# Kernel tuning notes

Hardware: AMD Instinct MI355X
Metric: run time of the kernel (lower is better)

The kernel has to match this reference:

```python
import jax, jax.numpy as jnp
import numpy as np

NUM_SAMPLES = 8192   # num_parallel_samples
HIDDEN = 512
EMB = 40             # embedding_dim(10) * freq_map['H'](4)
C_IN = 1
TIME_FEAT = 4
HIST_LEN = 336
PRED_LEN = 48
MIN_SCALE = 1e-5
SAMPLE_KEY_SEED = 42


def _gru_cell(h, x, W_ih, W_hh, b_ih, b_hh):
    # torch GRU cell: gates stacked as [r, z, n] along rows of W (each HIDDEN)
    gi = x @ W_ih.T + b_ih            # [B, 3H]
    gh = h @ W_hh.T + b_hh            # [B, 3H]
    H = h.shape[-1]
    i_r, i_z, i_n = gi[:, :H], gi[:, H:2 * H], gi[:, 2 * H:]
    h_r, h_z, h_n = gh[:, :H], gh[:, H:2 * H], gh[:, 2 * H:]
    r = jax.nn.sigmoid(i_r + h_r)
    z = jax.nn.sigmoid(i_z + h_z)
    n = jnp.tanh(i_n + r * h_n)
    return (1.0 - z) * n + z * h


def setup_inputs() -> dict:
    key = jax.random.key(0)
    ks = jax.random.split(key, 16)
    f32 = jnp.float32
    inp = {
        "x": jax.random.normal(ks[0], (1, HIST_LEN, C_IN), dtype=f32),
        "x_mark": jax.random.normal(ks[1], (1, HIST_LEN, TIME_FEAT), dtype=f32),
        "y_mark": jax.random.normal(ks[2], (1, PRED_LEN, TIME_FEAT), dtype=f32),
        "mode": 0,
        # time_feat_embedding: Linear(4 -> 40), torch layout [out, in]
        "W_emb": jax.random.normal(ks[3], (EMB, TIME_FEAT), dtype=f32) * 0.05,
        "b_emb": jnp.zeros((EMB,), dtype=f32),
        # GRU (1 layer): input size = c_in + EMB = 41
        "W_ih": jax.random.normal(ks[4], (3 * HIDDEN, C_IN + EMB), dtype=f32) * 0.05,
        "W_hh": jax.random.normal(ks[5], (3 * HIDDEN, HIDDEN), dtype=f32) * 0.05,
        "b_ih": jnp.zeros((3 * HIDDEN,), dtype=f32),
        "b_hh": jnp.zeros((3 * HIDDEN,), dtype=f32),
        # StudentT args projection: three Linear(HIDDEN -> 1)
        "W_df": jax.random.normal(ks[6], (1, HIDDEN), dtype=f32) * 0.05,
        "b_df": jnp.zeros((1,), dtype=f32),
        "W_loc": jax.random.normal(ks[7], (1, HIDDEN), dtype=f32) * 0.05,
        "b_loc": jnp.zeros((1,), dtype=f32),
        "W_sc": jax.random.normal(ks[8], (1, HIDDEN), dtype=f32) * 0.05,
        "b_sc": jnp.zeros((1,), dtype=f32),
    }
    return inp


def _deepar_sample(x, x_mark, y_mark, W_emb, b_emb, W_ih, W_hh, b_ih, b_hh,
                   W_df, b_df, W_loc, b_loc, W_sc, b_sc):
    S = NUM_SAMPLES
    # ---- encoder (unroll_encoder with y=None) ----
    scale = jnp.clip(jnp.mean(jnp.abs(x), axis=1, keepdims=True), MIN_SCALE, None)  # [1,1,1]
    seq = x / scale
    tfe = x_mark @ W_emb.T + b_emb                      # [1, T, EMB]
    enc_in = jnp.concatenate([seq, tfe], axis=-1)       # [1, T, 41]
    h0 = jnp.zeros((1, HIDDEN), dtype=x.dtype)

    def enc_step(h, xt):  # xt: [1, 41]
        h = _gru_cell(h, xt, W_ih, W_hh, b_ih, b_hh)
        return h, None

    h_T, _ = jax.lax.scan(enc_step, h0, jnp.swapaxes(enc_in, 0, 1))  # [1, H]

    # ---- sampling decoder ----
    h = jnp.broadcast_to(h_T, (S, HIDDEN))              # repeat state across samples
    # note: original feeds the UNSCALED last observation as first decoder input
    tgt0 = jnp.broadcast_to(x[0, -1, :], (S, C_IN))     # [S, 1]
    emb_y = y_mark[0] @ W_emb.T + b_emb                 # [pred_len, EMB]
    scale_s = scale[0, 0, 0]                            # scalar (batch=1, c=1)
    base_key = jax.random.key(SAMPLE_KEY_SEED)

    def dec_step(carry, xs):
        h, tgt = carry
        e_k, k = xs
        inp = jnp.concatenate([tgt, jnp.broadcast_to(e_k, (S, EMB))], axis=-1)  # [S, 41]
        h = _gru_cell(h, inp, W_ih, W_hh, b_ih, b_hh)
        # StudentTOutput domain map: df = 2 + softplus, loc raw, scale = softplus
        df = 2.0 + jax.nn.softplus(h @ W_df.T + b_df)   # [S, 1]
        loc = h @ W_loc.T + b_loc                       # [S, 1]
        sc = jax.nn.softplus(h @ W_sc.T + b_sc)         # [S, 1]
        eps = jax.random.t(jax.random.fold_in(base_key, k),
                           jax.lax.stop_gradient(df), df.shape, dtype=df.dtype)
        sample = (loc + sc * eps) * scale_s             # AffineTransformed(scale)
        return (h, sample), sample

    ks = jnp.arange(PRED_LEN)
    _, samples = jax.lax.scan(dec_step, (h, tgt0), (emb_y, ks))  # [pred_len, S, 1]
    return jnp.transpose(samples, (1, 0, 2))            # [S, pred_len, c_out]


def reference(x, x_mark, y_mark, mode, W_emb, b_emb, W_ih, W_hh, b_ih, b_hh,
              W_df, b_df, W_loc, b_loc, W_sc, b_sc):
    # mode=0 -> sampling/inference path (the kernel target)
    return _deepar_sample(x, x_mark, y_mark, W_emb, b_emb, W_ih, W_hh, b_ih, b_hh,
                          W_df, b_df, W_loc, b_loc, W_sc, b_sc)
```

## Files before the change

### kernel.cpp

```cpp
#include <hip/hip_runtime.h>
#include <cmath>


#define JAX_PARTITIONABLE 1

#define HIDDEN 512
#define EMB 40
#define HIST 336
#define PRED 48
#define S_N 8192
#define ENC_BLOCKS 48

#define HPLANE (8192 * 512)
#define WPLANE (1536 * 512)
#define INV4096 (1.0f / 4096.0f)

typedef __attribute__((ext_vector_type(8))) _Float16 half8;
typedef __attribute__((ext_vector_type(4))) float f32x4;

struct KeyPair { unsigned a, b; };

__device__ __forceinline__ unsigned rotl32_(unsigned v, unsigned s) {
  return (v << s) | (v >> (32u - s));
}

__device__ __forceinline__ KeyPair tf2x32(KeyPair k, unsigned x0, unsigned x1) {
  unsigned ks0 = k.a, ks1 = k.b, ks2 = ks0 ^ ks1 ^ 0x1BD11BDAu;
  x0 += ks0; x1 += ks1;
#define TF_R(r) { x0 += x1; x1 = rotl32_(x1, r); x1 ^= x0; }
  TF_R(13u) TF_R(15u) TF_R(26u) TF_R(6u)  x0 += ks1; x1 += ks2 + 1u;
  TF_R(17u) TF_R(29u) TF_R(16u) TF_R(24u) x0 += ks2; x1 += ks0 + 2u;
  TF_R(13u) TF_R(15u) TF_R(26u) TF_R(6u)  x0 += ks0; x1 += ks1 + 3u;
  TF_R(17u) TF_R(29u) TF_R(16u) TF_R(24u) x0 += ks1; x1 += ks2 + 4u;
  TF_R(13u) TF_R(15u) TF_R(26u) TF_R(6u)  x0 += ks2; x1 += ks0 + 5u;
#undef TF_R
  KeyPair r; r.a = x0; r.b = x1; return r;
}

__device__ __forceinline__ void split2_(KeyPair key, KeyPair& r0, KeyPair& r1) {
#if JAX_PARTITIONABLE
  r0 = tf2x32(key, 0u, 0u);
  r1 = tf2x32(key, 0u, 1u);
#else
  KeyPair p0 = tf2x32(key, 0u, 2u);
  KeyPair p1 = tf2x32(key, 1u, 3u);
  r0.a = p0.a; r0.b = p1.a;
  r1.a = p0.b; r1.b = p1.b;
#endif
}

__device__ __forceinline__ void split3_(KeyPair key, KeyPair& r0, KeyPair& r1, KeyPair& r2) {
#if JAX_PARTITIONABLE
  r0 = tf2x32(key, 0u, 0u);
  r1 = tf2x32(key, 0u, 1u);
  r2 = tf2x32(key, 0u, 2u);
#else
  KeyPair p0 = tf2x32(key, 0u, 3u);
  KeyPair p1 = tf2x32(key, 1u, 4u);
  KeyPair p2 = tf2x32(key, 2u, 5u);
  r0.a = p0.a; r0.b = p1.a;
  r1.a = p2.a; r1.b = p0.b;
  r2.a = p1.b; r2.b = p2.b;
#endif
}

__device__ __forceinline__ unsigned scalar_bits_(KeyPair key) {
#if JAX_PARTITIONABLE
  KeyPair p = tf2x32(key, 0u, 0u);
  return p.a ^ p.b;
#else
  return tf2x32(key, 0u, 0u).a;
#endif
}

__device__ __forceinline__ unsigned batch_bits_8192_(KeyPair key, int s) {
#if JAX_PARTITIONABLE
  KeyPair p = tf2x32(key, 0u, (unsigned)s);
  return p.a ^ p.b;
#else
  if (s < 4096) return tf2x32(key, (unsigned)s, (unsigned)(4096 + s)).a;
  return tf2x32(key, (unsigned)(s - 4096), (unsigned)s).b;
#endif
}

__device__ __forceinline__ KeyPair subkey_of_8192_(KeyPair key, int s) {
#if JAX_PARTITIONABLE
  return tf2x32(key, 0u, (unsigned)s);
#else
  KeyPair r;
  if (s < 4096) {
    r.a = tf2x32(key, (unsigned)(2 * s),     (unsigned)(8192 + 2 * s)).a;
    r.b = tf2x32(key, (unsigned)(2 * s + 1), (unsigned)(8192 + 2 * s + 1)).a;
  } else {
    int m = 2 * s - 8192;
    r.a = tf2x32(key, (unsigned)m,       (unsigned)(m + 8192)).b;
    r.b = tf2x32(key, (unsigned)(m + 1), (unsigned)(m + 1 + 8192)).b;
  }
  return r;
#endif
}

__device__ __forceinline__ float acc_logf_(float x) {
  return (float)log((double)x);
}
__device__ __forceinline__ float acc_expf_(float x) {
  return (float)exp((double)x);
}

__device__ __forceinline__ float bits_to_uniform01_(unsigned bits) {
  return __uint_as_float((bits >> 9) | 0x3F800000u) - 1.0f;
}

__device__ __forceinline__ float xla_log1pf_(float t) {
  #pragma clang fp contract(off)
  float small_ = (1.0f + (-0.5f) * t) * t;
  float large_ = acc_logf_(t + 1.0f);
  return (fabsf(t) < 1e-4f) ? small_ : large_;
}

__device__ float xla_erfinv_(float x) {
  #pragma clang fp contract(off)
  float w = -xla_log1pf_(-(x * x));
  float p;
  if (w < 5.0f) {
    float ww = w - 2.5f;
    p = 2.81022636e-08f;
    p = 3.43273939e-07f + p * ww;
    p = -3.5233877e-06f + p * ww;
    p = -4.39150654e-06f + p * ww;
    p = 0.00021858087f + p * ww;
    p = -0.00125372503f + p * ww;
    p = -0.00417768164f + p * ww;
    p = 0.246640727f + p * ww;
    p = 1.50140941f + p * ww;
  } else {
    float ww = sqrtf(w) - 3.0f;
    p = -0.000200214257f;
    p = 0.000100950558f + p * ww;
    p = 0.00134934322f + p * ww;
    p = -0.00367342844f + p * ww;
    p = 0.00573950773f + p * ww;
    p = -0.0076224613f + p * ww;
    p = 0.00943887047f + p * ww;
    p = 1.00167406f + p * ww;
    p = 2.83297682f + p * ww;
  }
  return p * x;
}

__device__ float bits_to_normal_(unsigned bits) {
  #pragma clang fp contract(off)
  const float lo = __uint_as_float(0xBF7FFFFFu);
  float f = bits_to_uniform01_(bits);
  float u = f * 2.0f + lo;
  u = fmaxf(lo, u);
  return __uint_as_float(0x3FB504F3u) * xla_erfinv_(u);
}

__device__ __forceinline__ float softplus_(float x) {
  #pragma clang fp contract(off)
  float amax = fmaxf(x, 0.0f);
  float e = acc_expf_(-fabsf(x));
  return amax + xla_log1pf_(e);
}

__device__ __forceinline__ float sigmoid_(float v) { return 1.0f / (1.0f + expf(-v)); }

__device__ __forceinline__ unsigned short f2h_(float f) {
  _Float16 h = (_Float16)f;
  return __builtin_bit_cast(unsigned short, h);
}
__device__ __forceinline__ float h2f_(unsigned short b) {
  return (float)__builtin_bit_cast(_Float16, b);
}

__device__ float gamma_sample_(KeyPair gkey, float alpha) {
  #pragma clang fp contract(off)
  const float third = 0.33333334f;
  float d = alpha - third;
  float c = third / sqrtf(d);
  KeyPair key, boost_sub;
  split2_(gkey, key, boost_sub);
  (void)boost_sub;
  float X = 0.0f, V = 1.0f, U = 2.0f;
  for (int guard = 0; guard < 1024; guard++) {
    float X2 = X * X;
    float sq = 1.0f - 0.0331f * (X2 * X2);
    bool cont = false;
    if (U >= sq) {
      float lhs = acc_logf_(U);
      float rhs = (X * 0.5f) + (d * ((1.0f - V) + acc_logf_(V)));
      cont = (lhs >= rhs);
    }
    if (!cont) break;
    KeyPair nkey, xkey, Ukey;
    split3_(key, nkey, xkey, Ukey);
    key = nkey;
    float x, v;
    KeyPair kk = xkey;
    do {
      KeyPair knew, sub;
      split2_(kk, knew, sub);
      kk = knew;
      x = bits_to_normal_(scalar_bits_(sub));
      v = 1.0f + x * c;
    } while (v <= 0.0f);
    X = x * x;
    V = (v * v) * v;
    U = bits_to_uniform01_(scalar_bits_(Ukey));
  }
  return d * V;
}

__device__ float sample_t_eps_(int k, int s, float df) {
  #pragma clang fp contract(off)
  KeyPair base; base.a = 0u; base.b = 42u;
  KeyPair tkey = tf2x32(base, 0u, (unsigned)k);
  KeyPair key_n, key_g;
  split2_(tkey, key_n, key_g);
  float n = bits_to_normal_(batch_bits_8192_(key_n, s));
  KeyPair gkey = subkey_of_8192_(key_g, s);
  float half_df = df * 0.5f;
  float g = gamma_sample_(gkey, half_df);
  return n * sqrtf(half_df / g);
}


__global__ __launch_bounds__(256) void prep_kernel(
    const float* __restrict__ x, const float* __restrict__ x_mark,
    const float* __restrict__ y_mark, const float* __restrict__ W_emb,
    const float* __restrict__ b_emb, float* __restrict__ scale_p,
    float* __restrict__ tfe, float* __restrict__ emb_y,
    unsigned* __restrict__ flags) {
  int tid = threadIdx.x;
  if (tid == 0) {
    float s = 0.0f;
    for (int t = 0; t < HIST; t++) s += fabsf(x[t]);
    float m = s / 336.0f;
    scale_p[0] = fmaxf(m, 1e-5f);
  }
  for (int i = tid; i < ENC_BLOCKS * 16; i += 256) flags[i] = 0u;
  for (int idx = tid; idx < HIST * EMB; idx += 256) {
    int t = idx / EMB, e = idx % EMB;
    float a = b_emb[e];
    for (int f = 0; f < 4; f++) a += x_mark[t * 4 + f] * W_emb[e * 4 + f];
    tfe[idx] = a;
  }
  for (int idx = tid; idx < PRED * EMB; idx += 256) {
    int kk = idx / EMB, e = idx % EMB;
    float a = b_emb[e];
    for (int f = 0; f < 4; f++) a += y_mark[kk * 4 + f] * W_emb[e * 4 + f];
    emb_y[idx] = a;
  }
}

__global__ __launch_bounds__(256) void enc_gi_kernel(
    const float* __restrict__ x, const float* __restrict__ tfe,
    const float* __restrict__ W_ih, const float* __restrict__ b_ih,
    const float* __restrict__ scale_p, float* __restrict__ enc_gi) {
  __shared__ float fe[EMB];
  __shared__ float xs_s;
  int t = blockIdx.x;
  int tid = threadIdx.x;
  if (tid < EMB) fe[tid] = tfe[t * EMB + tid];
  if (tid == 0) xs_s = x[t] / scale_p[0];
  __syncthreads();
  float xs = xs_s;
  for (int r = tid; r < 3 * HIDDEN; r += 256) {
    const float* wr = W_ih + (size_t)r * 41;
    float a = b_ih[r] + wr[0] * xs;
    #pragma unroll
    for (int e = 0; e < EMB; e++) a += wr[1 + e] * fe[e];
    enc_gi[(size_t)t * 1536 + r] = a;
  }
}

__global__ __launch_bounds__(256) void giy_kernel(
    const float* __restrict__ emb_y, const float* __restrict__ W_ih,
    const float* __restrict__ b_ih, float* __restrict__ giy) {
  __shared__ float fe[EMB];
  int k = blockIdx.x;
  int tid = threadIdx.x;
  if (tid < EMB) fe[tid] = emb_y[k * EMB + tid];
  __syncthreads();
  for (int r = tid; r < 3 * HIDDEN; r += 256) {
    const float* wr = W_ih + (size_t)r * 41;
    float a = b_ih[r];
    #pragma unroll
    for (int e = 0; e < EMB; e++) a += wr[1 + e] * fe[e];
    giy[(size_t)k * 1536 + r] = a;
  }
}

__global__ __launch_bounds__(256) void wsplit_kernel(
    const float* __restrict__ W_hh, unsigned short* __restrict__ Wr) {
  int row = blockIdx.x;
  int g = row >> 9;
  int jg = row & 511;
  int jb = jg >> 5, jl = jg & 31;
  size_t dst = ((size_t)jb * 96 + g * 32 + jl) * 512;
  for (int k = threadIdx.x; k < 512; k += 256) {
    float w = W_hh[(size_t)row * 512 + k];
    unsigned short g0 = f2h_(w);
    float r1 = (w - h2f_(g0)) * 4096.0f;
    unsigned short g1 = f2h_(r1);
    Wr[dst + k] = g0;
    Wr[WPLANE + dst + k] = g1;
  }
}

__global__ __launch_bounds__(256) void hsplit_kernel(
    const float* __restrict__ h_T, unsigned short* __restrict__ sT) {
  int i = threadIdx.x;
  for (int j = i; j < 512; j += 256) {
    float v = h_T[j];
    unsigned short f0 = f2h_(v);
    float r1 = (v - h2f_(f0)) * 4096.0f;
    sT[j] = f0;
    sT[512 + j] = f2h_(r1);
  }
}

__global__ __launch_bounds__(128) void h2bcast_kernel(
    const unsigned short* __restrict__ sT, unsigned short* __restrict__ h2) {
  int row = blockIdx.x;
  int tid = threadIdx.x;
  int sp = tid >> 6, c = tid & 63;
  ((uint4*)(h2 + (size_t)sp * HPLANE + (size_t)row * 512))[c] =
      ((const uint4*)(sT + sp * 512))[c];
}

__global__ __launch_bounds__(256) void enc_gru_kernel(
    const float* __restrict__ enc_gi, const float* __restrict__ W_hh,
    const float* __restrict__ b_hh, float* __restrict__ ghbuf,
    unsigned* __restrict__ flags, float* __restrict__ h_T) {
  __shared__ __align__(16) float hs[HIDDEN];
  int tid = threadIdx.x;
  int gtid = blockIdx.x * 256 + tid;
  int row = gtid >> 3;
  int sub = gtid & 7;

  float w[64];
  const float* wp = W_hh + (size_t)row * HIDDEN + sub * 64;
  #pragma unroll
  for (int i = 0; i < 16; i++) {
    float4 v = *(const float4*)(wp + 4 * i);
    w[4 * i + 0] = v.x; w[4 * i + 1] = v.y; w[4 * i + 2] = v.z; w[4 * i + 3] = v.w;
  }
  if (tid < 128) *(float4*)&hs[tid * 4] = make_float4(0.f, 0.f, 0.f, 0.f);
  float bhr0 = b_hh[tid],       bhz0 = b_hh[512 + tid],  bhn0 = b_hh[1024 + tid];
  float bhr1 = b_hh[256 + tid], bhz1 = b_hh[768 + tid],  bhn1 = b_hh[1280 + tid];
  __syncthreads();

  for (int t = 0; t < HIST; t++) {
    float p = 0.0f;
    const float4* hv = (const float4*)&hs[sub * 64];
    #pragma unroll
    for (int i = 0; i < 16; i++) {
      float4 v = hv[i];
      p += w[4 * i + 0] * v.x + w[4 * i + 1] * v.y +
           w[4 * i + 2] * v.z + w[4 * i + 3] * v.w;
    }
    p += __shfl_xor(p, 1, 64);
    p += __shfl_xor(p, 2, 64);
    p += __shfl_xor(p, 4, 64);
    int par = t & 1;
    if (sub == 0)
      __hip_atomic_store(&ghbuf[par * 1536 + row], p, __ATOMIC_RELAXED,
                         __HIP_MEMORY_SCOPE_AGENT);
    __syncthreads();
    if (tid == 0)
      __hip_atomic_store(&flags[blockIdx.x * 16], (unsigned)(t + 1),
                         __ATOMIC_RELEASE, __HIP_MEMORY_SCOPE_AGENT);
    if (tid < ENC_BLOCKS) {
      while (__hip_atomic_load(&flags[tid * 16], __ATOMIC_ACQUIRE,
                               __HIP_MEMORY_SCOPE_AGENT) < (unsigned)(t + 1))
        __builtin_amdgcn_s_sleep(1);
    }
    __syncthreads();
    float hn0, hn1;
    {
      int j = tid;
      float ghr = __hip_atomic_load(&ghbuf[par * 1536 + j], __ATOMIC_RELAXED, __HIP_MEMORY_SCOPE_AGENT);
      float ghz = __hip_atomic_load(&ghbuf[par * 1536 + 512 + j], __ATOMIC_RELAXED, __HIP_MEMORY_SCOPE_AGENT);
      float ghn = __hip_atomic_load(&ghbuf[par * 1536 + 1024 + j], __ATOMIC_RELAXED, __HIP_MEMORY_SCOPE_AGENT);
      float gir = enc_gi[(size_t)t * 1536 + j];
      float giz = enc_gi[(size_t)t * 1536 + 512 + j];
      float gin = enc_gi[(size_t)t * 1536 + 1024 + j];
      float r = sigmoid_(gir + (ghr + bhr0));
      float z = sigmoid_(giz + (ghz + bhz0));
      float n = tanhf(gin + r * (ghn + bhn0));
      hn0 = (1.0f - z) * n + z * hs[j];
    }
    {
      int j = tid + 256;
      float ghr = __hip_atomic_load(&ghbuf[par * 1536 + j], __ATOMIC_RELAXED, __HIP_MEMORY_SCOPE_AGENT);
      float ghz = __hip_atomic_load(&ghbuf[par * 1536 + 512 + j], __ATOMIC_RELAXED, __HIP_MEMORY_SCOPE_AGENT);
      float ghn = __hip_atomic_load(&ghbuf[par * 1536 + 1024 + j], __ATOMIC_RELAXED, __HIP_MEMORY_SCOPE_AGENT);
      float gir = enc_gi[(size_t)t * 1536 + j];
      float giz = enc_gi[(size_t)t * 1536 + 512 + j];
      float gin = enc_gi[(size_t)t * 1536 + 1024 + j];
      float r = sigmoid_(gir + (ghr + bhr1));
      float z = sigmoid_(giz + (ghz + bhz1));
      float n = tanhf(gin + r * (ghn + bhn1));
      hn1 = (1.0f - z) * n + z * hs[j];
    }
    hs[tid] = hn0;
    hs[tid + 256] = hn1;
    __syncthreads();
  }
  if (blockIdx.x == 0 && tid < 128)
    *(float4*)&h_T[tid * 4] = *(float4*)&hs[tid * 4];
}

__global__ __launch_bounds__(256, 2) void dec_gru_mfma(
    const unsigned short* __restrict__ h2_in,
    const unsigned short* __restrict__ Wr,
    const float* __restrict__ giy_k, const float* __restrict__ b_hh,
    const float* __restrict__ W_ih, const float* __restrict__ tgt,
    int tgt_is_x, unsigned short* __restrict__ h2_out,
    const float* __restrict__ W_df, const float* __restrict__ W_loc,
    const float* __restrict__ W_sc, float* __restrict__ partials) {
  __shared__ unsigned short As[2][2][128][32];
  int b_ = blockIdx.x;
  int xcd = b_ & 7, slot = b_ >> 3;
  int mb = xcd * 8 + (slot & 7);
  int jb = slot >> 3;
  int tid = threadIdx.x;
  int lane = tid & 63;
  int wave = tid >> 6;
  int wm = wave >> 1, wn = wave & 1;
  int s0 = mb * 128;
  int q = lane >> 4, c = lane & 15;

  f32x4 accm[4][3], accc[4][3];
  #pragma unroll
  for (int i = 0; i < 4; i++)
    #pragma unroll
    for (int g = 0; g < 3; g++) {
      accm[i][g] = (f32x4){0.f, 0.f, 0.f, 0.f};
      accc[i][g] = (f32x4){0.f, 0.f, 0.f, 0.f};
    }

  float hold[4][4];
  #pragma unroll
  for (int i = 0; i < 4; i++)
    #pragma unroll
    for (int r = 0; r < 4; r++) hold[i][r] = 0.f;

  int asp[4], arow[4], acol[4];
  #pragma unroll
  for (int r = 0; r < 4; r++) {
    int a = r * 256 + tid;
    asp[r] = a >> 9;
    int rem = a & 511;
    arow[r] = rem >> 2;
    acol[r] = rem & 3;
  }

  const unsigned short* Bbase =
      Wr + ((size_t)jb * 96 + wn * 16 + c) * 512 + q * 8;

  #pragma unroll
  for (int r = 0; r < 4; r++) {
    uint4 v = *(const uint4*)(h2_in + (size_t)asp[r] * HPLANE +
                              (size_t)(s0 + arow[r]) * 512 + acol[r] * 8);
    *(uint4*)&As[0][asp[r]][arow[r]][(acol[r] ^ (arow[r] & 3)) * 8] = v;
  }
  half8 Bcur[3][2];
  #pragma unroll
  for (int g = 0; g < 3; g++) {
    Bcur[g][0] = *(const half8*)(Bbase + (size_t)g * 32 * 512);
    Bcur[g][1] = *(const half8*)(Bbase + WPLANE + (size_t)g * 32 * 512);
  }
  __syncthreads();

  int cur = 0;
  for (int kbi = 0; kbi < 16; kbi++) {
    int kb = kbi * 32;
    uint4 Areg[4];
    half8 Bn[3][2];
    if (kbi < 15) {
      #pragma unroll
      for (int r = 0; r < 4; r++)
        Areg[r] = *(const uint4*)(h2_in + (size_t)asp[r] * HPLANE +
                                  (size_t)(s0 + arow[r]) * 512 + kb + 32 +
                                  acol[r] * 8);
      #pragma unroll
      for (int g = 0; g < 3; g++) {
        Bn[g][0] = *(const half8*)(Bbase + (size_t)g * 32 * 512 + kb + 32);
        Bn[g][1] = *(const half8*)(Bbase + WPLANE + (size_t)g * 32 * 512 + kb + 32);
      }
    }
    if (kbi == jb) {
      int cc = wn * 16 + c;
      #pragma unroll
      for (int i = 0; i < 4; i++)
        #pragma unroll
        for (int reg = 0; reg < 4; reg++) {
          int m = wm * 64 + i * 16 + q * 4 + reg;
          int idx = (((cc >> 3) ^ (m & 3)) << 3) + (cc & 7);
          hold[i][reg] = h2f_(As[cur][0][m][idx]) +
                         h2f_(As[cur][1][m][idx]) * INV4096;
        }
    }
    #pragma unroll
    for (int i = 0; i < 4; i++) {
      int m = wm * 64 + i * 16 + c;
      half8 a0 = *(const half8*)&As[cur][0][m][(q ^ (c & 3)) * 8];
      half8 a1 = *(const half8*)&As[cur][1][m][(q ^ (c & 3)) * 8];
      #pragma unroll
      for (int g = 0; g < 3; g++) {
        accm[i][g] = __builtin_amdgcn_mfma_f32_16x16x32_f16(a0, Bcur[g][0], accm[i][g], 0, 0, 0);
        accc[i][g] = __builtin_amdgcn_mfma_f32_16x16x32_f16(a0, Bcur[g][1], accc[i][g], 0, 0, 0);
        accc[i][g] = __builtin_amdgcn_mfma_f32_16x16x32_f16(a1, Bcur[g][0], accc[i][g], 0, 0, 0);
      }
    }
    if (kbi < 15) {
      #pragma unroll
      for (int r = 0; r < 4; r++)
        *(uint4*)&As[cur ^ 1][asp[r]][arow[r]][(acol[r] ^ (arow[r] & 3)) * 8] =
            Areg[r];
      #pragma unroll
      for (int g = 0; g < 3; g++) {
        Bcur[g][0] = Bn[g][0];
        Bcur[g][1] = Bn[g][1];
      }
    }
    __syncthreads();
    cur ^= 1;
  }

  float* pb = (float*)&As[0][0][0][0];
  {
    int j = jb * 32 + wn * 16 + c;
    float gyr = giy_k[j], gyz = giy_k[512 + j], gyn = giy_k[1024 + j];
    float w0r = W_ih[(size_t)j * 41];
    float w0z = W_ih[(size_t)(512 + j) * 41];
    float w0n = W_ih[(size_t)(1024 + j) * 41];
    float bhr = b_hh[j], bhz = b_hh[512 + j], bhn = b_hh[1024 + j];
    float wdj = W_df[j], wlj = W_loc[j], wsj = W_sc[j];
    #pragma unroll
    for (int i = 0; i < 4; i++) {
      #pragma unroll
      for (int reg = 0; reg < 4; reg++) {
        int s = s0 + wm * 64 + i * 16 + q * 4 + reg;
        float tg = tgt_is_x ? tgt[HIST - 1] : tgt[s];
        size_t off = (size_t)s * 512 + j;
        float h_old = hold[i][reg];
        float ghr = accm[i][0][reg] + accc[i][0][reg] * INV4096;
        float ghz = accm[i][1][reg] + accc[i][1][reg] * INV4096;
        float ghn = accm[i][2][reg] + accc[i][2][reg] * INV4096;
        float gr = (gyr + w0r * tg) + (ghr + bhr);
        float gz = (gyz + w0z * tg) + (ghz + bhz);
        float gn_i = gyn + w0n * tg;
        float gn_h = ghn + bhn;
        float r_ = sigmoid_(gr);
        float z_ = sigmoid_(gz);
        float n_ = tanhf(gn_i + r_ * gn_h);
        float hn = (1.0f - z_) * n_ + z_ * h_old;
        unsigned short f0 = f2h_(hn);
        float r1 = (hn - h2f_(f0)) * 4096.0f;
        __builtin_nontemporal_store(f0, &h2_out[off]);
        __builtin_nontemporal_store(f2h_(r1), &h2_out[HPLANE + off]);
        float vd = hn * wdj, vl = hn * wlj, vs = hn * wsj;
        #pragma unroll
        for (int o = 1; o < 16; o <<= 1) {
          vd += __shfl_xor(vd, o, 64);
          vl += __shfl_xor(vl, o, 64);
          vs += __shfl_xor(vs, o, 64);
        }
        if (c == 0) {
          int sl = i * 16 + q * 4 + reg;
          int bix = ((wm * 2 + wn) * 64 + sl) * 3;
          pb[bix + 0] = vd; pb[bix + 1] = vl; pb[bix + 2] = vs;
        }
      }
    }
  }
  __syncthreads();
  if (tid < 128) {
    int wmh = tid >> 6, sl = tid & 63;
    int ia = (wmh * 2 + 0) * 192 + sl * 3;
    int ib = ia + 192;
    int s = s0 + wmh * 64 + sl;
    size_t pofs = (size_t)s * 48 + jb * 3;
    partials[pofs + 0] = pb[ia + 0] + pb[ib + 0];
    partials[pofs + 1] = pb[ia + 1] + pb[ib + 1];
    partials[pofs + 2] = pb[ia + 2] + pb[ib + 2];
  }
}

__global__ __launch_bounds__(64) void dec_head_kernel(
    const float* __restrict__ partials, const float* __restrict__ b_df,
    const float* __restrict__ b_loc, const float* __restrict__ b_sc,
    const float* __restrict__ scale_p, float* __restrict__ tgt,
    float* __restrict__ out, int k) {
  #pragma clang fp contract(off)
  int s = blockIdx.x * 64 + threadIdx.x;
  const float* p = partials + (size_t)s * 48;
  float adf = 0.f, alo = 0.f, asc = 0.f;
  #pragma unroll
  for (int jb = 0; jb < 16; jb++) {
    adf += p[jb * 3 + 0];
    alo += p[jb * 3 + 1];
    asc += p[jb * 3 + 2];
  }
  float df = 2.0f + softplus_(adf + b_df[0]);
  float loc = alo + b_loc[0];
  float sc = softplus_(asc + b_sc[0]);
  float eps = sample_t_eps_(k, s, df);
  float smp = (loc + sc * eps) * scale_p[0];
  out[(size_t)s * PRED + k] = smp;
  tgt[s] = smp;
}

extern "C" void kernel_launch(void* const* d_in, const int* in_sizes, int n_in,
                              void* d_out, int out_size, void* d_ws, size_t ws_size,
                              hipStream_t stream) {
  const float* x      = (const float*)d_in[0];
  const float* x_mark = (const float*)d_in[1];
  const float* y_mark = (const float*)d_in[2];
  const float* W_emb  = (const float*)d_in[4];
  const float* b_emb  = (const float*)d_in[5];
  const float* W_ih   = (const float*)d_in[6];
  const float* W_hh   = (const float*)d_in[7];
  const float* b_ih   = (const float*)d_in[8];
  const float* b_hh   = (const float*)d_in[9];
  const float* W_df   = (const float*)d_in[10];
  const float* b_df   = (const float*)d_in[11];
  const float* W_loc  = (const float*)d_in[12];
  const float* b_loc  = (const float*)d_in[13];
  const float* W_sc   = (const float*)d_in[14];
  const float* b_sc   = (const float*)d_in[15];
  float* out = (float*)d_out;

  float* w = (float*)d_ws;
  unsigned short* h2_a = (unsigned short*)(w);
  unsigned short* h2_b = (unsigned short*)(w + 4194304);
  unsigned short* Wr   = (unsigned short*)(w + 8388608);
  float* enc_gi = w + 9175040;
  float* giy    = w + 9691136;
  float* tfe    = w + 9764864;
  float* emb_y  = w + 9778304;
  float* ghbuf  = w + 9780224;
  float* h_T    = w + 9783296;
  unsigned short* sT = (unsigned short*)(w + 9783808);
  float* tgt    = w + 9784320;
  float* scale_p = w + 9792512;
  unsigned* flags = (unsigned*)(w + 9792516);
  float* partials = w + 9793540;

  prep_kernel<<<1, 256, 0, stream>>>(x, x_mark, y_mark, W_emb, b_emb,
                                     scale_p, tfe, emb_y, flags);
  enc_gi_kernel<<<HIST, 256, 0, stream>>>(x, tfe, W_ih, b_ih, scale_p, enc_gi);
  giy_kernel<<<PRED, 256, 0, stream>>>(emb_y, W_ih, b_ih, giy);
  wsplit_kernel<<<1536, 256, 0, stream>>>(W_hh, Wr);
  enc_gru_kernel<<<ENC_BLOCKS, 256, 0, stream>>>(enc_gi, W_hh, b_hh, ghbuf,
                                                 flags, h_T);
  hsplit_kernel<<<1, 256, 0, stream>>>(h_T, sT);
  h2bcast_kernel<<<S_N, 128, 0, stream>>>(sT, h2_a);

  for (int k = 0; k < PRED; k++) {
    const unsigned short* h_in = (k % 2 == 0) ? h2_a : h2_b;
    unsigned short* h_o = (k % 2 == 0) ? h2_b : h2_a;
    dec_gru_mfma<<<1024, 256, 0, stream>>>(
        h_in, Wr, giy + (size_t)k * 1536, b_hh, W_ih,
        (k == 0) ? x : tgt, (k == 0) ? 1 : 0, h_o,
        W_df, W_loc, W_sc, partials);
    dec_head_kernel<<<S_N / 64, 64, 0, stream>>>(
        partials, b_df, b_loc, b_sc, scale_p, tgt, out, k);
  }
}
```

Measured before the change: 5.617 ms.

## Fuse all decoder timesteps into one persistent kernel with LDS-resident hidden state

Result: slower. 10.19 ms (+81.3%).

```diff
diff --git a/kernel.cpp b/kernel.cpp
--- a/kernel.cpp
+++ b/kernel.cpp
@@ -11,7 +11,6 @@
 #define S_N 8192
 #define ENC_BLOCKS 48
 
-#define HPLANE (8192 * 512)
 #define WPLANE (1536 * 512)
 #define INV4096 (1.0f / 4096.0f)
 
@@ -321,22 +320,15 @@
   }
 }
 
-__global__ __launch_bounds__(128) void h2bcast_kernel(
-    const unsigned short* __restrict__ sT, unsigned short* __restrict__ h2) {
-  int row = blockIdx.x;
-  int tid = threadIdx.x;
-  int sp = tid >> 6, c = tid & 63;
-  ((uint4*)(h2 + (size_t)sp * HPLANE + (size_t)row * 512))[c] =
-      ((const uint4*)(sT + sp * 512))[c];
-}
-
 __global__ __launch_bounds__(256) void enc_gru_kernel(
     const float* __restrict__ enc_gi, const float* __restrict__ W_hh,
     const float* __restrict__ b_hh, float* __restrict__ ghbuf,
     unsigned* __restrict__ flags, float* __restrict__ h_T) {
+  if (blockIdx.x & 7) return;
+  int blk = blockIdx.x >> 3;
   __shared__ __align__(16) float hs[HIDDEN];
   int tid = threadIdx.x;
-  int gtid = blockIdx.x * 256 + tid;
+  int gtid = blk * 256 + tid;
   int row = gtid >> 3;
   int sub = gtid & 7;
 
@@ -370,7 +362,7 @@
                          __HIP_MEMORY_SCOPE_AGENT);
     __syncthreads();
     if (tid == 0)
-      __hip_atomic_store(&flags[blockIdx.x * 16], (unsigned)(t + 1),
+      __hip_atomic_store(&flags[blk * 16], (unsigned)(t + 1),
                          __ATOMIC_RELEASE, __HIP_MEMORY_SCOPE_AGENT);
     if (tid < ENC_BLOCKS) {
       while (__hip_atomic_load(&flags[tid * 16], __ATOMIC_ACQUIRE,
@@ -409,210 +401,198 @@
     hs[tid + 256] = hn1;
     __syncthreads();
   }
-  if (blockIdx.x == 0 && tid < 128)
+  if (blk == 0 && tid < 128)
     *(float4*)&h_T[tid * 4] = *(float4*)&hs[tid * 4];
 }
 
-__global__ __launch_bounds__(256, 2) void dec_gru_mfma(
-    const unsigned short* __restrict__ h2_in,
-    const unsigned short* __restrict__ Wr,
-    const float* __restrict__ giy_k, const float* __restrict__ b_hh,
-    const float* __restrict__ W_ih, const float* __restrict__ tgt,
-    int tgt_is_x, unsigned short* __restrict__ h2_out,
-    const float* __restrict__ W_df, const float* __restrict__ W_loc,
-    const float* __restrict__ W_sc, float* __restrict__ partials) {
-  __shared__ unsigned short As[2][2][128][32];
-  int b_ = blockIdx.x;
-  int xcd = b_ & 7, slot = b_ >> 3;
-  int mb = xcd * 8 + (slot & 7);
-  int jb = slot >> 3;
+__global__ __launch_bounds__(256, 1) void dec_fused(
+    const unsigned short* __restrict__ sT, const unsigned short* __restrict__ Wr,
+    const float* __restrict__ giy, const float* __restrict__ b_hh,
+    const float* __restrict__ W_ih, const float* __restrict__ x,
+    const float* __restrict__ W_df, const float* __restrict__ b_df,
+    const float* __restrict__ W_loc, const float* __restrict__ b_loc,
+    const float* __restrict__ W_sc, const float* __restrict__ b_sc,
+    const float* __restrict__ scale_p, float* __restrict__ out) {
+  __shared__ __align__(16) unsigned short hb[2][2][32][512];
+  __shared__ float pbuf[16][32][3];
+  __shared__ float tgt_l[32];
   int tid = threadIdx.x;
   int lane = tid & 63;
   int wave = tid >> 6;
-  int wm = wave >> 1, wn = wave & 1;
-  int s0 = mb * 128;
   int q = lane >> 4, c = lane & 15;
-
-  f32x4 accm[4][3], accc[4][3];
-  #pragma unroll
-  for (int i = 0; i < 4; i++)
+  int s0 = blockIdx.x * 32;
+
+  float xlast = x[HIST - 1];
+  float scale = scale_p[0];
+
+  if (tid < 32) tgt_l[tid] = xlast;
+  for (int idx = tid; idx < 1024; idx += 256) {
+    int sp = idx >> 9, kk = idx & 511;
+    unsigned short v = sT[sp * 512 + kk];
+    int ch = kk >> 3, e = kk & 7;
     #pragma unroll
-    for (int g = 0; g < 3; g++) {
-      accm[i][g] = (f32x4){0.f, 0.f, 0.f, 0.f};
-      accc[i][g] = (f32x4){0.f, 0.f, 0.f, 0.f};
-    }
-
-  float hold[4][4];
-  #pragma unroll
-  for (int i = 0; i < 4; i++)
-    #pragma unroll
-    for (int r = 0; r < 4; r++) hold[i][r] = 0.f;
-
-  int asp[4], arow[4], acol[4];
-  #pragma unroll
-  for (int r = 0; r < 4; r++) {
-    int a = r * 256 + tid;
-    asp[r] = a >> 9;
-    int rem = a & 511;
-    arow[r] = rem >> 2;
-    acol[r] = rem & 3;
-  }
-
-  const unsigned short* Bbase =
-      Wr + ((size_t)jb * 96 + wn * 16 + c) * 512 + q * 8;
-
-  #pragma unroll
-  for (int r = 0; r < 4; r++) {
-    uint4 v = *(const uint4*)(h2_in + (size_t)asp[r] * HPLANE +
-                              (size_t)(s0 + arow[r]) * 512 + acol[r] * 8);
-    *(uint4*)&As[0][asp[r]][arow[r]][(acol[r] ^ (arow[r] & 3)) * 8] = v;
-  }
-  half8 Bcur[3][2];
-  #pragma unroll
-  for (int g = 0; g < 3; g++) {
-    Bcur[g][0] = *(const half8*)(Bbase + (size_t)g * 32 * 512);
-    Bcur[g][1] = *(const half8*)(Bbase + WPLANE + (size_t)g * 32 * 512);
+    for (int s = 0; s < 32; s++)
+      hb[0][sp][s][((ch ^ (s & 7)) << 3) | e] = v;
   }
   __syncthreads();
 
-  int cur = 0;
-  for (int kbi = 0; kbi < 16; kbi++) {
-    int kb = kbi * 32;
-    uint4 Areg[4];
-    half8 Bn[3][2];
-    if (kbi < 15) {
+  for (int k = 0; k < PRED; k++) {
+    int cur = k & 1, nxt = cur ^ 1;
+    const float* giy_k = giy + (size_t)k * 1536;
+
+    for (int jj = 0; jj < 4; jj++) {
+      int jb = wave * 4 + jj;
+
+      const unsigned short* Brow[6];
       #pragma unroll
-      for (int r = 0; r < 4; r++)
-        Areg[r] = *(const uint4*)(h2_in + (size_t)asp[r] * HPLANE +
-                                  (size_t)(s0 + arow[r]) * 512 + kb + 32 +
-                                  acol[r] * 8);
+      for (int n = 0; n < 6; n++) {
+        int row = jb * 96 + (n >> 1) * 32 + (n & 1) * 16 + c;
+        Brow[n] = Wr + (size_t)row * 512 + q * 8;
+      }
+
+      f32x4 am[2][6], ac[2][6];
       #pragma unroll
-      for (int g = 0; g < 3; g++) {
-        Bn[g][0] = *(const half8*)(Bbase + (size_t)g * 32 * 512 + kb + 32);
-        Bn[g][1] = *(const half8*)(Bbase + WPLANE + (size_t)g * 32 * 512 + kb + 32);
+      for (int mt = 0; mt < 2; mt++)
+        #pragma unroll
+        for (int n = 0; n < 6; n++) {
+          am[mt][n] = (f32x4){0.f, 0.f, 0.f, 0.f};
+          ac[mt][n] = (f32x4){0.f, 0.f, 0.f, 0.f};
+        }
+
+      half8 Ah[2][2], An[2][2], Bc[6][2], Bn[6][2];
+      #pragma unroll
+      for (int mt = 0; mt < 2; mt++) {
+        int m = mt * 16 + c;
+        int off = (((0 * 4 + q) ^ (m & 7)) << 3);
+        Ah[mt][0] = *(const half8*)&hb[cur][0][m][off];
+        Ah[mt][1] = *(const half8*)&hb[cur][1][m][off];
+      }
+      #pragma unroll
+      for (int n = 0; n < 6; n++) {
+        Bc[n][0] = *(const half8*)(Brow[n]);
+        Bc[n][1] = *(const half8*)(Brow[n] + WPLANE);
+      }
+
+      for (int kbi = 0; kbi < 16; kbi++) {
+        if (kbi < 15) {
+          #pragma unroll
+          for (int mt = 0; mt < 2; mt++) {
+            int m = mt * 16 + c;
+            int off = ((((kbi + 1) * 4 + q) ^ (m & 7)) << 3);
+            An[mt][0] = *(const half8*)&hb[cur][0][m][off];
+            An[mt][1] = *(const half8*)&hb[cur][1][m][off];
+          }
+          #pragma unroll
+          for (int n = 0; n < 6; n++) {
+            Bn[n][0] = *(const half8*)(Brow[n] + (kbi + 1) * 32);
+            Bn[n][1] = *(const half8*)(Brow[n] + WPLANE + (kbi + 1) * 32);
+          }
+        }
+        #pragma unroll
+        for (int mt = 0; mt < 2; mt++) {
+          #pragma unroll
+          for (int n = 0; n < 6; n++) {
+            am[mt][n] = __builtin_amdgcn_mfma_f32_16x16x32_f16(Ah[mt][0], Bc[n][0], am[mt][n], 0, 0, 0);
+            ac[mt][n] = __builtin_amdgcn_mfma_f32_16x16x32_f16(Ah[mt][0], Bc[n][1], ac[mt][n], 0, 0, 0);
+            ac[mt][n] = __builtin_amdgcn_mfma_f32_16x16x32_f16(Ah[mt][1], Bc[n][0], ac[mt][n], 0, 0, 0);
+          }
+        }
+        if (kbi < 15) {
+          #pragma unroll
+          for (int mt = 0; mt < 2; mt++) {
+            Ah[mt][0] = An[mt][0];
+            Ah[mt][1] = An[mt][1];
+          }
+          #pragma unroll
+          for (int n = 0; n < 6; n++) {
+            Bc[n][0] = Bn[n][0];
+            Bc[n][1] = Bn[n][1];
+          }
+        }
+      }
+
+      float gy[2][3], w0[2][3], bh[2][3], wh[2][3];
+      #pragma unroll
+      for (int jt = 0; jt < 2; jt++) {
+        int j = jb * 32 + jt * 16 + c;
+        gy[jt][0] = giy_k[j]; gy[jt][1] = giy_k[512 + j]; gy[jt][2] = giy_k[1024 + j];
+        w0[jt][0] = W_ih[(size_t)j * 41];
+        w0[jt][1] = W_ih[(size_t)(512 + j) * 41];
+        w0[jt][2] = W_ih[(size_t)(1024 + j) * 41];
+        bh[jt][0] = b_hh[j]; bh[jt][1] = b_hh[512 + j]; bh[jt][2] = b_hh[1024 + j];
+        wh[jt][0] = W_df[j]; wh[jt][1] = W_loc[j]; wh[jt][2] = W_sc[j];
+      }
+      #pragma unroll
+      for (int mt = 0; mt < 2; mt++) {
+        #pragma unroll
+        for (int reg = 0; reg < 4; reg++) {
+          int s = mt * 16 + q * 4 + reg;
+          float tg = tgt_l[s];
+          float vdt[2], vlt[2], vst[2];
+          #pragma unroll
+          for (int jt = 0; jt < 2; jt++) {
+            int n0 = jt, n1 = 2 + jt, n2 = 4 + jt;
+            int j = jb * 32 + jt * 16 + c;
+            int swz = (((j >> 3) ^ (s & 7)) << 3) | (j & 7);
+            float h_old = h2f_(hb[cur][0][s][swz]) +
+                          h2f_(hb[cur][1][s][swz]) * INV4096;
+            float ghr = am[mt][n0][reg] + ac[mt][n0][reg] * INV4096;
+            float ghz = am[mt][n1][reg] + ac[mt][n1][reg] * INV4096;
+            float ghn = am[mt][n2][reg] + ac[mt][n2][reg] * INV4096;
+            float gr = (gy[jt][0] + w0[jt][0] * tg) + (ghr + bh[jt][0]);
+            float gz = (gy[jt][1] + w0[jt][1] * tg) + (ghz + bh[jt][1]);
+            float gn_i = gy[jt][2] + w0[jt][2] * tg;
+            float gn_h = ghn + bh[jt][2];
+            float r_ = sigmoid_(gr);
+            float z_ = sigmoid_(gz);
+            float n_ = tanhf(gn_i + r_ * gn_h);
+            float hn = (1.0f - z_) * n_ + z_ * h_old;
+            unsigned short f0 = f2h_(hn);
+            float r1 = (hn - h2f_(f0)) * 4096.0f;
+            hb[nxt][0][s][swz] = f0;
+            hb[nxt][1][s][swz] = f2h_(r1);
+            float vd = hn * wh[jt][0], vl = hn * wh[jt][1], vs = hn * wh[jt][2];
+            #pragma unroll
+            for (int o = 1; o < 16; o <<= 1) {
+              vd += __shfl_xor(vd, o, 64);
+              vl += __shfl_xor(vl, o, 64);
+              vs += __shfl_xor(vs, o, 64);
+            }
+            vdt[jt] = vd; vlt[jt] = vl; vst[jt] = vs;
+          }
+          if (c == 0) {
+            pbuf[jb][s][0] = vdt[0] + vdt[1];
+            pbuf[jb][s][1] = vlt[0] + vlt[1];
+            pbuf[jb][s][2] = vst[0] + vst[1];
+          }
+        }
       }
     }
-    if (kbi == jb) {
-      int cc = wn * 16 + c;
-      #pragma unroll
-      for (int i = 0; i < 4; i++)
+
+    __syncthreads();
+
+    {
+      #pragma clang fp contract(off)
+      if (lane < 8) {
+        int sl = wave * 8 + lane;
+        float adf = 0.f, alo = 0.f, asc = 0.f;
         #pragma unroll
-        for (int reg = 0; reg < 4; reg++) {
-          int m = wm * 64 + i * 16 + q * 4 + reg;
-          int idx = (((cc >> 3) ^ (m & 3)) << 3) + (cc & 7);
-          hold[i][reg] = h2f_(As[cur][0][m][idx]) +
-                         h2f_(As[cur][1][m][idx]) * INV4096;
+        for (int jb = 0; jb < 16; jb++) {
+          adf += pbuf[jb][sl][0];
+          alo += pbuf[jb][sl][1];
+          asc += pbuf[jb][sl][2];
         }
-    }
-    #pragma unroll
-    for (int i = 0; i < 4; i++) {
-      int m = wm * 64 + i * 16 + c;
-      half8 a0 = *(const half8*)&As[cur][0][m][(q ^ (c & 3)) * 8];
-      half8 a1 = *(const half8*)&As[cur][1][m][(q ^ (c & 3)) * 8];
-      #pragma unroll
-      for (int g = 0; g < 3; g++) {
-        accm[i][g] = __builtin_amdgcn_mfma_f32_16x16x32_f16(a0, Bcur[g][0], accm[i][g], 0, 0, 0);
-        accc[i][g] = __builtin_amdgcn_mfma_f32_16x16x32_f16(a0, Bcur[g][1], accc[i][g], 0, 0, 0);
-        accc[i][g] = __builtin_amdgcn_mfma_f32_16x16x32_f16(a1, Bcur[g][0], accc[i][g], 0, 0, 0);
-      }
-    }
-    if (kbi < 15) {
-      #pragma unroll
-      for (int r = 0; r < 4; r++)
-        *(uint4*)&As[cur ^ 1][asp[r]][arow[r]][(acol[r] ^ (arow[r] & 3)) * 8] =
-            Areg[r];
-      #pragma unroll
-      for (int g = 0; g < 3; g++) {
-        Bcur[g][0] = Bn[g][0];
-        Bcur[g][1] = Bn[g][1];
+        float df = 2.0f + softplus_(adf + b_df[0]);
+        float loc = alo + b_loc[0];
+        float sc = softplus_(asc + b_sc[0]);
+        float eps = sample_t_eps_(k, s0 + sl, df);
+        float smp = (loc + sc * eps) * scale;
+        out[(size_t)(s0 + sl) * PRED + k] = smp;
+        tgt_l[sl] = smp;
       }
     }
     __syncthreads();
-    cur ^= 1;
-  }
-
-  float* pb = (float*)&As[0][0][0][0];
-  {
-    int j = jb * 32 + wn * 16 + c;
-    float gyr = giy_k[j], gyz = giy_k[512 + j], gyn = giy_k[1024 + j];
-    float w0r = W_ih[(size_t)j * 41];
-    float w0z = W_ih[(size_t)(512 + j) * 41];
-    float w0n = W_ih[(size_t)(1024 + j) * 41];
-    float bhr = b_hh[j], bhz = b_hh[512 + j], bhn = b_hh[1024 + j];
-    float wdj = W_df[j], wlj = W_loc[j], wsj = W_sc[j];
-    #pragma unroll
-    for (int i = 0; i < 4; i++) {
-      #pragma unroll
-      for (int reg = 0; reg < 4; reg++) {
-        int s = s0 + wm * 64 + i * 16 + q * 4 + reg;
-        float tg = tgt_is_x ? tgt[HIST - 1] : tgt[s];
-        size_t off = (size_t)s * 512 + j;
-        float h_old = hold[i][reg];
-        float ghr = accm[i][0][reg] + accc[i][0][reg] * INV4096;
-        float ghz = accm[i][1][reg] + accc[i][1][reg] * INV4096;
-        float ghn = accm[i][2][reg] + accc[i][2][reg] * INV4096;
-        float gr = (gyr + w0r * tg) + (ghr + bhr);
-        float gz = (gyz + w0z * tg) + (ghz + bhz);
-        float gn_i = gyn + w0n * tg;
-        float gn_h = ghn + bhn;
-        float r_ = sigmoid_(gr);
-        float z_ = sigmoid_(gz);
-        float n_ = tanhf(gn_i + r_ * gn_h);
-        float hn = (1.0f - z_) * n_ + z_ * h_old;
-        unsigned short f0 = f2h_(hn);
-        float r1 = (hn - h2f_(f0)) * 4096.0f;
-        __builtin_nontemporal_store(f0, &h2_out[off]);
-        __builtin_nontemporal_store(f2h_(r1), &h2_out[HPLANE + off]);
-        float vd = hn * wdj, vl = hn * wlj, vs = hn * wsj;
-        #pragma unroll
-        for (int o = 1; o < 16; o <<= 1) {
-          vd += __shfl_xor(vd, o, 64);
-          vl += __shfl_xor(vl, o, 64);
-          vs += __shfl_xor(vs, o, 64);
-        }
-        if (c == 0) {
-          int sl = i * 16 + q * 4 + reg;
-          int bix = ((wm * 2 + wn) * 64 + sl) * 3;
-          pb[bix + 0] = vd; pb[bix + 1] = vl; pb[bix + 2] = vs;
-        }
-      }
-    }
-  }
-  __syncthreads();
-  if (tid < 128) {
-    int wmh = tid >> 6, sl = tid & 63;
-    int ia = (wmh * 2 + 0) * 192 + sl * 3;
-    int ib = ia + 192;
-    int s = s0 + wmh * 64 + sl;
-    size_t pofs = (size_t)s * 48 + jb * 3;
-    partials[pofs + 0] = pb[ia + 0] + pb[ib + 0];
-    partials[pofs + 1] = pb[ia + 1] + pb[ib + 1];
-    partials[pofs + 2] = pb[ia + 2] + pb[ib + 2];
-  }
-}
-
-__global__ __launch_bounds__(64) void dec_head_kernel(
-    const float* __restrict__ partials, const float* __restrict__ b_df,
-    const float* __restrict__ b_loc, const float* __restrict__ b_sc,
-    const float* __restrict__ scale_p, float* __restrict__ tgt,
-    float* __restrict__ out, int k) {
-  #pragma clang fp contract(off)
-  int s = blockIdx.x * 64 + threadIdx.x;
-  const float* p = partials + (size_t)s * 48;
-  float adf = 0.f, alo = 0.f, asc = 0.f;
-  #pragma unroll
-  for (int jb = 0; jb < 16; jb++) {
-    adf += p[jb * 3 + 0];
-    alo += p[jb * 3 + 1];
-    asc += p[jb * 3 + 2];
-  }
-  float df = 2.0f + softplus_(adf + b_df[0]);
-  float loc = alo + b_loc[0];
-  float sc = softplus_(asc + b_sc[0]);
-  float eps = sample_t_eps_(k, s, df);
-  float smp = (loc + sc * eps) * scale_p[0];
-  out[(size_t)s * PRED + k] = smp;
-  tgt[s] = smp;
+  }
 }
 
 extern "C" void kernel_launch(void* const* d_in, const int* in_sizes, int n_in,
@@ -636,39 +616,27 @@
   float* out = (float*)d_out;
 
   float* w = (float*)d_ws;
-  unsigned short* h2_a = (unsigned short*)(w);
-  unsigned short* h2_b = (unsigned short*)(w + 4194304);
-  unsigned short* Wr   = (unsigned short*)(w + 8388608);
-  float* enc_gi = w + 9175040;
-  float* giy    = w + 9691136;
-  float* tfe    = w + 9764864;
-  float* emb_y  = w + 9778304;
-  float* ghbuf  = w + 9780224;
-  float* h_T    = w + 9783296;
-  unsigned short* sT = (unsigned short*)(w + 9783808);
-  float* tgt    = w + 9784320;
-  float* scale_p = w + 9792512;
-  unsigned* flags = (unsigned*)(w + 9792516);
-  float* partials = w + 9793540;
+  unsigned short* Wr = (unsigned short*)(w);
+  float* enc_gi = w + 393216;
+  float* giy    = w + 909312;
+  float* tfe    = w + 983040;
+  float* emb_y  = w + 996480;
+  float* ghbuf  = w + 998400;
+  float* h_T    = w + 1001472;
+  unsigned short* sT = (unsigned short*)(w + 1001984);
+  float* scale_p = w + 1002496;
+  unsigned* flags = (unsigned*)(w + 1002500);
 
   prep_kernel<<<1, 256, 0, stream>>>(x, x_mark, y_mark, W_emb, b_emb,
                                      scale_p, tfe, emb_y, flags);
   enc_gi_kernel<<<HIST, 256, 0, stream>>>(x, tfe, W_ih, b_ih, scale_p, enc_gi);
   giy_kernel<<<PRED, 256, 0, stream>>>(emb_y, W_ih, b_ih, giy);
   wsplit_kernel<<<1536, 256, 0, stream>>>(W_hh, Wr);
-  enc_gru_kernel<<<ENC_BLOCKS, 256, 0, stream>>>(enc_gi, W_hh, b_hh, ghbuf,
-                                                 flags, h_T);
+  enc_gru_kernel<<<ENC_BLOCKS * 8, 256, 0, stream>>>(enc_gi, W_hh, b_hh,
+                                                     ghbuf, flags, h_T);
   hsplit_kernel<<<1, 256, 0, stream>>>(h_T, sT);
-  h2bcast_kernel<<<S_N, 128, 0, stream>>>(sT, h2_a);
-
-  for (int k = 0; k < PRED; k++) {
-    const unsigned short* h_in = (k % 2 == 0) ? h2_a : h2_b;
-    unsigned short* h_o = (k % 2 == 0) ? h2_b : h2_a;
-    dec_gru_mfma<<<1024, 256, 0, stream>>>(
-        h_in, Wr, giy + (size_t)k * 1536, b_hh, W_ih,
-        (k == 0) ? x : tgt, (k == 0) ? 1 : 0, h_o,
-        W_df, W_loc, W_sc, partials);
-    dec_head_kernel<<<S_N / 64, 64, 0, stream>>>(
-        partials, b_df, b_loc, b_sc, scale_p, tgt, out, k);
-  }
-}
+
+  dec_fused<<<256, 256, 0, stream>>>(
+      sT, Wr, giy, b_hh, W_ih, x, W_df, b_df, W_loc, b_loc, W_sc, b_sc,
+      scale_p, out);
+}
```
